# Kernel optimization log

Measured on AMD Instinct MI355X. Metric: run time of the kernel, lower is better.

## Reference

```python
import jax, jax.numpy as jnp
import numpy as np
from jax import lax

D_MODEL = 1024
N_HEADS = 16
D_HEAD = D_MODEL // N_HEADS  # 64
NB_FEAT = 266
CHUNK = 128
KERNEL_EPS = 1e-4
CAUSAL_EPS = 1e-6


def _gaussian_orthogonal_matrix(nb_rows, nb_cols, seed=0):
    # Performer gaussian_orthogonal_random_matrix, scaling=0:
    # stacked orthogonal blocks scaled by chi-distributed row norms.
    rng = np.random.default_rng(seed)
    blocks = []
    n_full = nb_rows // nb_cols + (1 if nb_rows % nb_cols else 0)
    for _ in range(n_full):
        g = rng.standard_normal((nb_cols, nb_cols))
        q_mat, _ = np.linalg.qr(g)
        blocks.append(q_mat.T)
    mat = np.concatenate(blocks, axis=0)[:nb_rows]
    multiplier = np.linalg.norm(rng.standard_normal((nb_rows, nb_cols)), axis=1)
    return jnp.asarray((multiplier[:, None] * mat).astype(np.float32))


def setup_inputs() -> dict:
    key = jax.random.key(0)
    ks = jax.random.split(key, 9)
    s = 1.0 / np.sqrt(D_MODEL)
    x = jax.random.normal(ks[0], (2, 4096, D_MODEL), dtype=jnp.float32)
    def lin(k):
        kw, kb = jax.random.split(k)
        W = jax.random.uniform(kw, (D_MODEL, D_MODEL), jnp.float32, -s, s)
        b = jax.random.uniform(kb, (D_MODEL,), jnp.float32, -s, s)
        return W, b
    Wq, bq = lin(ks[1]); Wk, bk = lin(ks[2]); Wv, bv = lin(ks[3]); Wo, bo = lin(ks[4])
    proj = _gaussian_orthogonal_matrix(NB_FEAT, D_HEAD)
    return {"x": x, "Wq": Wq, "bq": bq, "Wk": Wk, "bk": bk, "Wv": Wv, "bv": bv,
            "Wo": Wo, "bo": bo, "proj": proj}


def _softmax_kernel(data, proj, is_query):
    # Performer random-feature softmax kernel.
    data_normalizer = data.shape[-1] ** -0.25
    ratio = proj.shape[0] ** -0.5
    dn = data * data_normalizer  # [b,h,n,d]
    data_dash = jnp.einsum('bhnd,md->bhnm', dn, proj)
    diag = 0.5 * jnp.sum(dn * dn, axis=-1, keepdims=True)  # [b,h,n,1]
    if is_query:
        stab = jnp.max(data_dash, axis=-1, keepdims=True)
    else:
        stab = jnp.max(data_dash)
    return ratio * (jnp.exp(data_dash - diag - stab) + KERNEL_EPS)


def _causal_linear_attention(qp, kp, v, chunk_size):
    # Chunked O(n) causal linear attention (Performer noncuda variant).
    b, h, n, m = qp.shape
    d = v.shape[-1]
    nc = n // chunk_size
    qc = jnp.moveaxis(qp.reshape(b, h, nc, chunk_size, m), 2, 0)  # [nc,b,h,c,m]
    kc = jnp.moveaxis(kp.reshape(b, h, nc, chunk_size, m), 2, 0)
    vc = jnp.moveaxis(v.reshape(b, h, nc, chunk_size, d), 2, 0)   # [nc,b,h,c,d]

    def step(carry, inp):
        last_k, last_ctx = carry  # [b,h,m], [b,h,m,d]
        q, k, vv = inp
        k_cum = last_k[:, :, None, :] + jnp.cumsum(k, axis=-2)          # [b,h,c,m]
        D_inv = 1.0 / jnp.einsum('bhcm,bhcm->bhc', q, k_cum + CAUSAL_EPS)
        ctx = jnp.einsum('bhcm,bhcd->bhcmd', k, vv)                     # [b,h,c,m,d]
        ctx_cum = last_ctx[:, :, None, :, :] + jnp.cumsum(ctx, axis=2)
        out = jnp.einsum('bhcmd,bhcm,bhc->bhcd', ctx_cum, q, D_inv)
        return (k_cum[:, :, -1, :], ctx_cum[:, :, -1, :, :]), out

    carry0 = (jnp.zeros((b, h, m), qp.dtype), jnp.zeros((b, h, m, d), qp.dtype))
    _, outs = lax.scan(step, carry0, (qc, kc, vc))  # [nc,b,h,c,d]
    return jnp.moveaxis(outs, 0, 2).reshape(b, h, n, d)


def reference(x, Wq, bq, Wk, bk, Wv, bv, Wo, bo, proj):
    bsz, n, _ = x.shape
    def split_heads(t):
        return t.reshape(bsz, n, N_HEADS, D_HEAD).transpose(0, 2, 1, 3)  # [b,h,n,d]
    q = split_heads(x @ Wq.T + bq)
    k = split_heads(x @ Wk.T + bk)
    v = split_heads(x @ Wv.T + bv)
    q_prime = _softmax_kernel(q, proj, is_query=True)
    k_prime = _softmax_kernel(k, proj, is_query=False)
    attn = _causal_linear_attention(q_prime, k_prime, v, CHUNK)  # [b,h,n,d]
    attn = attn.transpose(0, 2, 1, 3).reshape(bsz, n, D_MODEL)
    return attn @ Wo.T + bo
```

## Files before the change

### kernel.cpp

```cpp
#include <hip/hip_runtime.h>

#define B_    2
#define NSEQ  4096
#define DM    1024
#define H_    16
#define DH    64
#define MF    266
#define MP    288
#define NROWS (B_*NSEQ)
#define NHROWS (B_*H_*NSEQ)
#define RATIO 0.06131393394849658f
#define DNORM 0.3535533905932738f
#define KEPS  1e-4f
#define CEPS  1e-6f

#define CH    128
#define NC    32
#define SROW  (65*MP)
#define SELEM (64*MP)

#define AS1 __attribute__((address_space(1)))
#define AS3 __attribute__((address_space(3)))

typedef unsigned short u16;
typedef unsigned int   u32;

typedef __bf16 bf16x8 __attribute__((ext_vector_type(8)));
typedef float  f32x4  __attribute__((ext_vector_type(4)));

__device__ __forceinline__ float b2f(u16 u){ u32 x = ((u32)u) << 16; return __builtin_bit_cast(float, x); }
__device__ __forceinline__ u16 f2b(float f){
    u32 x = __builtin_bit_cast(u32, f);
    u32 r = x + 0x7fffu + ((x >> 16) & 1u);
    return (u16)(r >> 16);
}
__device__ __forceinline__ u32 enc_max(float f){ u32 b = __builtin_bit_cast(u32, f); return (b & 0x80000000u) ? ~b : (b | 0x80000000u); }
__device__ __forceinline__ float dec_max(u32 u){ u32 b = (u & 0x80000000u) ? (u & 0x7fffffffu) : ~u; return __builtin_bit_cast(float, b); }

struct DetectArgs { const u32* p[10]; int nw[10]; };

__global__ void detect_all(DetectArgs a, u32* __restrict__ flags)
{
    __shared__ int cnt[256];
    int k = blockIdx.x;
    const u32* src = a.p[k];
    int nwords = a.nw[k];
    int t = threadIdx.x; int c = 0;
    for (int i = t; i < nwords; i += 256) {
        u32 w = src[i];
        int ea = (int)((w >> 7)  & 0xFF);
        int eb = (int)((w >> 23) & 0xFF);
        c += (ea >= 112 && ea <= 143) ? 1 : 0;
        c += (eb >= 112 && eb <= 143) ? 1 : 0;
    }
    cnt[t] = c; __syncthreads();
    for (int s = 128; s; s >>= 1) { if (t < s) cnt[t] += cnt[t + s]; __syncthreads(); }
    if (t == 0) flags[k] = (cnt[0] >= (nwords * 3) / 2) ? 1u : 0u;
}

__device__ __forceinline__ void conv8(const void* src, u16* dst, int i, u32 flag)
{
    if (flag) {
        *(uint4*)(dst + i) = *(const uint4*)((const u16*)src + i);
    } else {
        const float* s = (const float*)src + i;
        u16 tmp[8];
        #pragma unroll
        for (int j = 0; j < 8; ++j) tmp[j] = f2b(s[j]);
        *(uint4*)(dst + i) = *(uint4*)tmp;
    }
}

struct ConvAllArgs {
    const void* xs;    u16* xd;
    const void* wsrc[4]; u16* wdst[4];
    const void* bsrc[4]; u16* bdst[4];
    const void* pj;    u16* pjd;
    u32* gpart; u32* gmax;
    const u32* flags;
};

__global__ __launch_bounds__(256)
void conv_all(ConvAllArgs a)
{
    int blk = blockIdx.x, t = threadIdx.x;
    if (blk < 4096) {
        int i = blk * 2048 + t * 8;
        conv8(a.xs, a.xd, i, a.flags[0]);
    } else if (blk < 6144) {
        int r = blk - 4096; int w = r >> 9; int i = (r & 511) * 2048 + t * 8;
        conv8(a.wsrc[w], a.wdst[w], i, a.flags[1 + 2*w]);
    } else if (blk < 6148) {
        int w = blk - 6144; int i = t * 8;
        if (i < DM) conv8(a.bsrc[w], a.bdst[w], i, a.flags[2 + 2*w]);
    } else if (blk < 6157) {
        int i = (blk - 6148) * 2048 + t * 8;
        if (i < MF * DH) conv8(a.pj, a.pjd, i, a.flags[9]);
        else             *(uint4*)(a.pjd + i) = (uint4){0,0,0,0};
    } else {
        a.gpart[t] = 0u;
        if (t == 0) *a.gmax = 0u;
    }
}

#define GEMM_BODY(A_, Bm_, bm_, bn_, ACC_)                                    \
    const int K = DM;                                                          \
    __shared__ u16 As[128 * 64];                                               \
    __shared__ u16 Bs[128 * 64];                                               \
    int t = threadIdx.x;                                                       \
    int wave = t >> 6, lane = t & 63;                                          \
    int wm = wave >> 1, wn = wave & 1;                                         \
    int quad = lane >> 4, l16 = lane & 15;                                     \
    int rowc = lane >> 3;                                                      \
    int csrc = ((lane & 7) ^ rowc) * 8;                                        \
    int cA = wave * 4;                                                         \
    const u16* ap0 = A_  + (size_t)(bm_ + cA*8 + rowc) * K + csrc;             \
    const u16* bp0 = Bm_ + (size_t)(bn_ + cA*8 + rowc) * K + csrc;             \
    u16* lA = As + cA * 512;                                                   \
    u16* lB = Bs + cA * 512;                                                   \
    f32x4 ACC_[4][4];                                                          \
    _Pragma("unroll")                                                          \
    for (int i = 0; i < 4; ++i)                                                \
        _Pragma("unroll")                                                      \
        for (int j = 0; j < 4; ++j) ACC_[i][j] = (f32x4){0.f,0.f,0.f,0.f};     \
    for (int k0 = 0; k0 < K; k0 += 64) {                                       \
        _Pragma("unroll")                                                      \
        for (int j = 0; j < 4; ++j) {                                          \
            __builtin_amdgcn_global_load_lds((const AS1 void*)(ap0 + (size_t)j*8*K + k0), (AS3 void*)(lA + j*512), 16, 0, 0); \
            __builtin_amdgcn_global_load_lds((const AS1 void*)(bp0 + (size_t)j*8*K + k0), (AS3 void*)(lB + j*512), 16, 0, 0); \
        }                                                                      \
        __syncthreads();                                                       \
        _Pragma("unroll")                                                      \
        for (int ks = 0; ks < 2; ++ks) {                                       \
            bf16x8 af[4], bfr[4];                                              \
            int sw = ((((ks << 2) | quad) ^ (l16 & 7)) << 4);                  \
            _Pragma("unroll")                                                  \
            for (int i = 0; i < 4; ++i) {                                      \
                af[i]  = *(const bf16x8*)((const char*)As + (wm*64 + i*16 + l16)*128 + sw); \
                bfr[i] = *(const bf16x8*)((const char*)Bs + (wn*64 + i*16 + l16)*128 + sw); \
            }                                                                  \
            _Pragma("unroll")                                                  \
            for (int i = 0; i < 4; ++i)                                        \
                _Pragma("unroll")                                              \
                for (int j = 0; j < 4; ++j)                                    \
                    ACC_[i][j] = __builtin_amdgcn_mfma_f32_16x16x32_bf16(af[i], bfr[j], ACC_[i][j], 0, 0, 0); \
        }                                                                      \
        __syncthreads();                                                       \
    }

__global__ __launch_bounds__(256)
void gemm_qkv(const u16* __restrict__ A,
              const u16* __restrict__ Wqb, const u16* __restrict__ Wkb,
              const u16* __restrict__ Wvb,
              const u16* __restrict__ bqb, const u16* __restrict__ bkb,
              const u16* __restrict__ bvb,
              u16* __restrict__ Vb, float* __restrict__ Qf, float* __restrict__ Kf)
{
    int bid = blockIdx.x;
    int xcd = bid & 7, pos = bid >> 3;
    int lb  = xcd * 192 + pos;
    int z   = lb >> 9;
    int q   = lb & 511;
    int idx = q & 15, sg = q >> 4;
    int sgm = sg & 15, sgn = sg >> 4;
    int bm = (sgm*4 + (idx & 3)) * 128;
    int bn = (sgn*4 + (idx >> 2)) * 128;

    const u16* Bm   = (z == 0) ? Wvb : (z == 1) ? Wqb : Wkb;
    const u16* bias = (z == 0) ? bvb : (z == 1) ? bqb : bkb;
    GEMM_BODY(A, Bm, bm, bn, acc)
    float* Of = (z == 1) ? Qf : Kf;
    #pragma unroll
    for (int i = 0; i < 4; ++i) {
        #pragma unroll
        for (int j = 0; j < 4; ++j) {
            int col = bn + wn*64 + j*16 + l16;
            float bv = b2f(bias[col]);
            #pragma unroll
            for (int r = 0; r < 4; ++r) {
                int row = bm + wm*64 + i*16 + quad*4 + r;
                float v = acc[i][j][r] + bv;
                if (z == 0) Vb[(size_t)row * DM + col] = f2b(v);
                else        Of[(size_t)row * DM + col] = v;
            }
        }
    }
}

template<int OUT_BF16>
__global__ __launch_bounds__(256)
void gemm_nt(const u16* __restrict__ A, const u16* __restrict__ Bm,
             const u16* __restrict__ bias, void* __restrict__ C)
{
    int bm = blockIdx.x * 128, bn = blockIdx.y * 128;
    GEMM_BODY(A, Bm, bm, bn, acc)
    #pragma unroll
    for (int i = 0; i < 4; ++i) {
        #pragma unroll
        for (int j = 0; j < 4; ++j) {
            int col = bn + wn*64 + j*16 + l16;
            float bv = b2f(bias[col]);
            #pragma unroll
            for (int r = 0; r < 4; ++r) {
                int row = bm + wm*64 + i*16 + quad*4 + r;
                float v = acc[i][j][r] + bv;
                if (OUT_BF16) ((u16*)C)[(size_t)row * DM + col] = f2b(v);
                else          ((float*)C)[(size_t)row * DM + col] = v;
            }
        }
    }
}

__global__ __launch_bounds__(256)
void feat_qk(const float* __restrict__ Xq, const float* __restrict__ Xk,
             const u16* __restrict__ projP, u16* __restrict__ Qp,
             u16* __restrict__ Kp, u32* __restrict__ gpart,
             float* __restrict__ lstab)
{
    int blk = blockIdx.x;
    int isK = blk >> 11;
    int blk2 = blk & 2047;
    int bh = blk2 >> 6, nt = blk2 & 63;
    int b = bh >> 4, h = bh & 15;
    int n0 = nt * 64;
    int t = threadIdx.x;
    int lane = t & 63, w = t >> 6;
    int quad = lane >> 4, l16 = lane & 15;

    const float* X = isK ? Xk : Xq;
    u16* OutP = isK ? Kp : Qp;

    __shared__ uint4 smemU[2368];
    __shared__ float red4[4];
    u16* smem16 = (u16*)smemU;

    const float* xrow = X + ((size_t)(b * NSEQ + n0 + w*16 + l16)) * DM + h * DH;
    float va[2][8];
    #pragma unroll
    for (int ks = 0; ks < 2; ++ks) {
        float4 u0 = *(const float4*)(xrow + ks*32 + quad*8);
        float4 u1 = *(const float4*)(xrow + ks*32 + quad*8 + 4);
        va[ks][0]=u0.x; va[ks][1]=u0.y; va[ks][2]=u0.z; va[ks][3]=u0.w;
        va[ks][4]=u1.x; va[ks][5]=u1.y; va[ks][6]=u1.z; va[ks][7]=u1.w;
    }

    for (int i = t; i < 2304; i += 256) {
        int m = i >> 3, c = i & 7;
        uint4 v = *(const uint4*)(projP + m*64 + c*8);
        int dstb = m*128 + ((c*16) ^ ((m & 7) << 4));
        *(uint4*)((char*)smemU + dstb) = v;
    }

    bf16x8 ahi[2], alo[2];
    float sq = 0.f;
    #pragma unroll
    for (int ks = 0; ks < 2; ++ks) {
        #pragma unroll
        for (int i = 0; i < 8; ++i) {
            float v = va[ks][i] * DNORM;
            sq += v * v;
            u16 hb = f2b(v);
            float hv = b2f(hb);
            ahi[ks][i] = __builtin_bit_cast(__bf16, hb);
            alo[ks][i] = __builtin_bit_cast(__bf16, f2b(v - hv));
        }
    }
    sq += __shfl_xor(sq, 16, 64);
    sq += __shfl_xor(sq, 32, 64);
    float diag_my = 0.5f * sq;

    __syncthreads();

    f32x4 acc[18];
    #pragma unroll
    for (int j = 0; j < 18; ++j) acc[j] = (f32x4){0.f,0.f,0.f,0.f};
    #pragma unroll
    for (int j = 0; j < 18; ++j) {
        int m = j*16 + l16;
        #pragma unroll
        for (int ks = 0; ks < 2; ++ks) {
            int off = m*128 + (((quad*16) + ks*64) ^ ((m & 7) << 4));
            bf16x8 bf = *(const bf16x8*)((const char*)smemU + off);
            acc[j] = __builtin_amdgcn_mfma_f32_16x16x32_bf16(ahi[ks], bf, acc[j], 0, 0, 0);
            acc[j] = __builtin_amdgcn_mfma_f32_16x16x32_bf16(alo[ks], bf, acc[j], 0, 0, 0);
        }
    }

    float rmax[4];
    #pragma unroll
    for (int r = 0; r < 4; ++r) rmax[r] = -3.4e38f;
    #pragma unroll
    for (int j = 0; j < 16; ++j)
        #pragma unroll
        for (int r = 0; r < 4; ++r) rmax[r] = fmaxf(rmax[r], acc[j][r]);
    if (l16 < MF - 256) {
        #pragma unroll
        for (int r = 0; r < 4; ++r) rmax[r] = fmaxf(rmax[r], acc[16][r]);
    }
    #pragma unroll
    for (int s = 1; s < 16; s <<= 1)
        #pragma unroll
        for (int r = 0; r < 4; ++r)
            rmax[r] = fmaxf(rmax[r], __shfl_xor(rmax[r], s, 64));

    float stab_blk = 0.f;
    if (isK) {
        float wm2 = fmaxf(fmaxf(rmax[0], rmax[1]), fmaxf(rmax[2], rmax[3]));
        wm2 = fmaxf(wm2, __shfl_xor(wm2, 16, 64));
        wm2 = fmaxf(wm2, __shfl_xor(wm2, 32, 64));
        if (lane == 0) red4[w] = wm2;
        __syncthreads();
        stab_blk = fmaxf(fmaxf(red4[0], red4[1]), fmaxf(red4[2], red4[3]));
        if (t == 0) {
            atomicMax(&gpart[blk2 & 255], enc_max(stab_blk));
            lstab[blk2] = stab_blk;
        }
    }

    float dg[4];
    #pragma unroll
    for (int r = 0; r < 4; ++r) dg[r] = __shfl(diag_my, quad*4 + r, 64);

    __syncthreads();

    #pragma unroll
    for (int j = 0; j < 18; ++j) {
        int m = j*16 + l16;
        #pragma unroll
        for (int r = 0; r < 4; ++r) {
            float stab = isK ? stab_blk : rmax[r];
            float ex = __expf(acc[j][r] - dg[r] - stab);
            float val = isK ? (RATIO * ex) : (RATIO * (ex + KEPS));
            u16 ov = (m < MF) ? f2b(val) : (u16)0;
            smem16[(w*16 + quad*4 + r) * 296 + m] = ov;
        }
    }
    __syncthreads();

    u16* obase = OutP + ((size_t)bh * NSEQ + n0) * MP;
    for (int i = t; i < 2304; i += 256) {
        int row = i / 36, c = i - row * 36;
        *(uint4*)(obase + row*MP + c*8) = *(const uint4*)(smem16 + row*296 + c*8);
    }
}

__global__ void gmax_reduce(const u32* __restrict__ gpart, u32* __restrict__ gmax)
{
    __shared__ u32 r[256];
    int t = threadIdx.x;
    r[t] = gpart[t]; __syncthreads();
    for (int s = 128; s; s >>= 1) { if (t < s) r[t] = max(r[t], r[t + s]); __syncthreads(); }
    if (t == 0) *gmax = r[0];
}

__global__ __launch_bounds__(256)
void krescale(u16* __restrict__ Kp, const float* __restrict__ lstab,
              const u32* __restrict__ gmax)
{
    int gid = blockIdx.x * 256 + threadIdx.x;
    int row = gid / 36, cc = gid - row * 36;
    float g = dec_max(*gmax);
    float sc = __expf(lstab[row >> 6] - g);
    u16* p = Kp + (size_t)row * MP + cc*8;
    uint4 v = *(uint4*)p;
    u16* e = (u16*)&v;
    int m0 = cc * 8;
    #pragma unroll
    for (int j = 0; j < 8; ++j) {
        float kv = b2f(e[j]) * sc + RATIO * KEPS;
        e[j] = (m0 + j < MF) ? f2b(kv) : (u16)0;
    }
    *(uint4*)p = v;
}

__global__ __launch_bounds__(256)
void chunk_ST(const u16* __restrict__ Kp, const u16* __restrict__ Vb,
              u16* __restrict__ Sb, float* __restrict__ zf)
{
    int bhc = blockIdx.x;
    int bh = bhc >> 5, c = bhc & (NC - 1);
    int b = bh >> 4, h = bh & 15;
    int t = threadIdx.x, w = t >> 6, lane = t & 63;
    int quad = lane >> 4, l16 = lane & 15;
    int n0 = c * CH;

    __shared__ __align__(16) u16 KTs[288*40];
    __shared__ __align__(16) u16 VTs[80*136];

    {
        int d0 = (t >> 5) * 8, nb = (t & 31) * 4;
        const u16* vb2 = Vb + ((size_t)(b*NSEQ + n0 + nb)) * DM + h*DH + d0;
        uint4 r0 = *(const uint4*)(vb2);
        uint4 r1 = *(const uint4*)(vb2 + DM);
        uint4 r2 = *(const uint4*)(vb2 + 2*DM);
        uint4 r3 = *(const uint4*)(vb2 + 3*DM);
        const u32* a0 = (const u32*)&r0; const u32* a1 = (const u32*)&r1;
        const u32* a2 = (const u32*)&r2; const u32* a3 = (const u32*)&r3;
        #pragma unroll
        for (int e = 0; e < 8; ++e) {
            u32 w0 = a0[e>>1], w1 = a1[e>>1], w2 = a2[e>>1], w3 = a3[e>>1];
            u32 lo2, hi2;
            if (e & 1) { lo2 = (w0 >> 16) | (w1 & 0xFFFF0000u); hi2 = (w2 >> 16) | (w3 & 0xFFFF0000u); }
            else       { lo2 = (w0 & 0xFFFFu) | (w1 << 16);     hi2 = (w2 & 0xFFFFu) | (w3 << 16); }
            uint2 uu; uu.x = lo2; uu.y = hi2;
            *(uint2*)&VTs[(d0 + e)*136 + nb] = uu;
        }
        if (t < 128) VTs[64*136 + t] = 0x3F80u;
        if (t < 255) {
            int rr = 65 + t/17, cc2 = t - (t/17)*17;
            uint4 z4 = (uint4){0,0,0,0};
            *(uint4*)&VTs[rr*136 + cc2*8] = z4;
        }
    }

    f32x4 am[18], az[5];
    #pragma unroll
    for (int mt = 0; mt < 18; ++mt) am[mt] = (f32x4){0.f,0.f,0.f,0.f};
    #pragma unroll
    for (int j = 0; j < 5; ++j) az[j] = (f32x4){0.f,0.f,0.f,0.f};

    const u16* kbase = Kp + ((size_t)bh * NSEQ + n0) * MP;
    for (int qh = 0; qh < 4; ++qh) {
        __syncthreads();
        for (int i = t; i < 288; i += 256) {
            int nb4 = (i & 7) * 4, m0 = (i >> 3) * 8;
            const u16* kb = kbase + (size_t)(qh*32 + nb4) * MP + m0;
            uint4 r0 = *(const uint4*)(kb);
            uint4 r1 = *(const uint4*)(kb + MP);
            uint4 r2 = *(const uint4*)(kb + 2*MP);
            uint4 r3 = *(const uint4*)(kb + 3*MP);
            const u32* a0 = (const u32*)&r0; const u32* a1 = (const u32*)&r1;
            const u32* a2 = (const u32*)&r2; const u32* a3 = (const u32*)&r3;
            #pragma unroll
            for (int e = 0; e < 8; ++e) {
                u32 w0 = a0[e>>1], w1 = a1[e>>1], w2 = a2[e>>1], w3 = a3[e>>1];
                u32 lo2, hi2;
                if (e & 1) { lo2 = (w0 >> 16) | (w1 & 0xFFFF0000u); hi2 = (w2 >> 16) | (w3 & 0xFFFF0000u); }
                else       { lo2 = (w0 & 0xFFFFu) | (w1 << 16);     hi2 = (w2 & 0xFFFFu) | (w3 << 16); }
                uint2 uu; uu.x = lo2; uu.y = hi2;
                *(uint2*)&KTs[(m0 + e)*40 + nb4] = uu;
            }
        }
        __syncthreads();
        int nof = qh*32 + quad*8;
        bf16x8 aw = *(const bf16x8*)&VTs[(w*16 + l16)*136 + nof];
        bf16x8 a4 = *(const bf16x8*)&VTs[(64 + l16)*136 + nof];
        #pragma unroll
        for (int mt = 0; mt < 18; ++mt) {
            bf16x8 bk = *(const bf16x8*)&KTs[(mt*16 + l16)*40 + quad*8];
            am[mt] = __builtin_amdgcn_mfma_f32_16x16x32_bf16(aw, bk, am[mt], 0, 0, 0);
        }
        #pragma unroll
        for (int j = 0; j < 5; ++j) {
            int mtz = w + 4*j;
            if (mtz < 18) {
                bf16x8 bk = *(const bf16x8*)&KTs[(mtz*16 + l16)*40 + quad*8];
                az[j] = __builtin_amdgcn_mfma_f32_16x16x32_bf16(a4, bk, az[j], 0, 0, 0);
            }
        }
    }

    u16* sb = Sb + (size_t)bhc * SELEM;
    #pragma unroll
    for (int mt = 0; mt < 18; ++mt)
        #pragma unroll
        for (int r = 0; r < 4; ++r)
            sb[(size_t)(w*16 + quad*4 + r) * MP + mt*16 + l16] = f2b(am[mt][r]);
    if (quad == 0) {
        #pragma unroll
        for (int j = 0; j < 5; ++j) {
            int mtz = w + 4*j;
            if (mtz < 18) zf[(size_t)bhc * MP + mtz*16 + l16] = az[j][0];
        }
    }
}

__global__ __launch_bounds__(256)
void chunk_prefix(u16* __restrict__ Sb, float* __restrict__ zf)
{
    int gid = blockIdx.x * 256 + threadIdx.x;
    int bh = gid / SROW;
    int rem = gid - bh * SROW;
    float run = 0.f;
    if (rem < SELEM) {
        size_t base = (size_t)(bh * NC) * SELEM + rem;
        #pragma unroll 4
        for (int c2 = 0; c2 < NC; ++c2) {
            size_t o = base + (size_t)c2 * SELEM;
            float v = b2f(Sb[o]);
            Sb[o] = f2b(run);
            run += v;
        }
    } else {
        int m = rem - SELEM;
        size_t base = (size_t)(bh * NC) * MP + m;
        #pragma unroll 4
        for (int c2 = 0; c2 < NC; ++c2) {
            size_t o = base + (size_t)c2 * MP;
            float v = zf[o];
            zf[o] = run + CEPS;
            run += v;
        }
    }
}

__global__ __launch_bounds__(256)
void scan_mfma(const u16* __restrict__ Qp, const u16* __restrict__ Kp,
               const u16* __restrict__ Vb, const u16* __restrict__ Sb,
               const float* __restrict__ zf, u16* __restrict__ attn)
{
    int bhc = blockIdx.x;
    int bh = bhc >> 5, c = bhc & (NC - 1);
    int b = bh >> 4, h = bh & 15;
    int t = threadIdx.x, w = t >> 6, lane = t & 63;
    int quad = lane >> 4, l16 = lane & 15;
    int n0 = c * CH;
    int it0 = w, it1 = 7 - w;

    __shared__ __align__(16) u16 R1s[9472];
    __shared__ __align__(16) u16 R2s[17408];

    for (int i = t; i < 2176; i += 256) ((uint4*)R2s)[i] = (uint4){0,0,0,0};

    bf16x8 q0[9], q1[9];
    {
        const u16* qa = Qp + ((size_t)bh * NSEQ + n0 + it0*16 + l16) * MP + quad*8;
        const u16* qb = Qp + ((size_t)bh * NSEQ + n0 + it1*16 + l16) * MP + quad*8;
        #pragma unroll
        for (int s = 0; s < 9; ++s) {
            q0[s] = *(const bf16x8*)(qa + s*32);
            q1[s] = *(const bf16x8*)(qb + s*32);
        }
    }

    float denw0 = 0.f, denw1 = 0.f;
    const u16* kbase = Kp + ((size_t)bh * NSEQ + n0) * MP;

    for (int qt = 0; qt < 4; ++qt) {
        __syncthreads();
        for (int i = t; i < 1152; i += 256) {
            int rr = i / 36, cc = i - rr * 36;
            *(uint4*)&R1s[rr*296 + cc*8] =
                *(const uint4*)(kbase + (size_t)(qt*32 + rr) * MP + cc*8);
        }
        __syncthreads();
        #pragma unroll
        for (int jj = 0; jj < 2; ++jj) {
            int jt = qt*2 + jj;
            #pragma unroll
            for (int itx = 0; itx < 2; ++itx) {
                int it = itx ? it1 : it0;
                if (jt <= it) {
                    f32x4 acc = (f32x4){0.f,0.f,0.f,0.f};
                    #pragma unroll
                    for (int s = 0; s < 9; ++s) {
                        bf16x8 kf = *(const bf16x8*)&R1s[(jj*16 + l16)*296 + s*32 + quad*8];
                        acc = __builtin_amdgcn_mfma_f32_16x16x32_bf16(
                            kf, itx ? q1[s] : q0[s], acc, 0, 0, 0);
                    }
                    int ig = it*16 + l16;
                    float rs = 0.f;
                    #pragma unroll
                    for (int r = 0; r < 4; ++r) {
                        int jg = jt*16 + quad*4 + r;
                        float pv = (jg <= ig) ? acc[r] : 0.f;
                        rs += pv;
                        R2s[ig*136 + jg] = f2b(pv);
                    }
                    if (itx) denw1 += rs; else denw0 += rs;
                }
            }
        }
    }

    __syncthreads();
    {
        int d0 = (t >> 5) * 8, nb = (t & 31) * 4;
        const u16* vb2 = Vb + ((size_t)(b*NSEQ + n0 + nb)) * DM + h*DH + d0;
        uint4 r0 = *(const uint4*)(vb2);
        uint4 r1 = *(const uint4*)(vb2 + DM);
        uint4 r2 = *(const uint4*)(vb2 + 2*DM);
        uint4 r3 = *(const uint4*)(vb2 + 3*DM);
        const u32* a0 = (const u32*)&r0; const u32* a1 = (const u32*)&r1;
        const u32* a2 = (const u32*)&r2; const u32* a3 = (const u32*)&r3;
        #pragma unroll
        for (int e = 0; e < 8; ++e) {
            u32 w0 = a0[e>>1], w1 = a1[e>>1], w2 = a2[e>>1], w3 = a3[e>>1];
            u32 lo2, hi2;
            if (e & 1) { lo2 = (w0 >> 16) | (w1 & 0xFFFF0000u); hi2 = (w2 >> 16) | (w3 & 0xFFFF0000u); }
            else       { lo2 = (w0 & 0xFFFFu) | (w1 << 16);     hi2 = (w2 & 0xFFFFu) | (w3 << 16); }
            uint2 uu; uu.x = lo2; uu.y = hi2;
            *(uint2*)&R1s[(d0 + e)*136 + nb] = uu;
        }
    }
    __syncthreads();

    f32x4 pacc[2][4];
    #pragma unroll
    for (int i = 0; i < 2; ++i)
        #pragma unroll
        for (int j = 0; j < 4; ++j) pacc[i][j] = (f32x4){0.f,0.f,0.f,0.f};
    int ns0 = (it0 + 2) >> 1, ns1 = (it1 + 2) >> 1;
    #pragma unroll
    for (int ks = 0; ks < 4; ++ks) {
        bool u0 = ks < ns0, u1 = ks < ns1;
        bf16x8 p0 = {}, p1 = {};
        if (u0) p0 = *(const bf16x8*)&R2s[(it0*16 + l16)*136 + ks*32 + quad*8];
        if (u1) p1 = *(const bf16x8*)&R2s[(it1*16 + l16)*136 + ks*32 + quad*8];
        #pragma unroll
        for (int ct = 0; ct < 4; ++ct) {
            bf16x8 vf = *(const bf16x8*)&R1s[(ct*16 + l16)*136 + ks*32 + quad*8];
            if (u0) pacc[0][ct] = __builtin_amdgcn_mfma_f32_16x16x32_bf16(p0, vf, pacc[0][ct], 0, 0, 0);
            if (u1) pacc[1][ct] = __builtin_amdgcn_mfma_f32_16x16x32_bf16(p1, vf, pacc[1][ct], 0, 0, 0);
        }
    }

    f32x4 cacc[2][4];
    #pragma unroll
    for (int i = 0; i < 2; ++i)
        #pragma unroll
        for (int j = 0; j < 4; ++j) cacc[i][j] = (f32x4){0.f,0.f,0.f,0.f};
    const u16* sbw = Sb + (size_t)bhc * SELEM;
    #pragma unroll
    for (int p = 0; p < 2; ++p) {
        __syncthreads();
        for (int i = t; i < 1152; i += 256) {
            int rr = i / 36, cc = i - rr * 36;
            *(uint4*)&R1s[rr*296 + cc*8] =
                *(const uint4*)(sbw + (size_t)(p*32 + rr) * MP + cc*8);
        }
        __syncthreads();
        #pragma unroll
        for (int s = 0; s < 9; ++s)
            #pragma unroll
            for (int cl = 0; cl < 2; ++cl) {
                bf16x8 sf = *(const bf16x8*)&R1s[(cl*16 + l16)*296 + s*32 + quad*8];
                cacc[0][p*2 + cl] = __builtin_amdgcn_mfma_f32_16x16x32_bf16(q0[s], sf, cacc[0][p*2 + cl], 0, 0, 0);
                cacc[1][p*2 + cl] = __builtin_amdgcn_mfma_f32_16x16x32_bf16(q1[s], sf, cacc[1][p*2 + cl], 0, 0, 0);
            }
    }

    float dc0 = 0.f, dc1 = 0.f;
    {
        const float* zc = zf + (size_t)bhc * MP + quad*8;
        #pragma unroll
        for (int s = 0; s < 9; ++s) {
            f32x4 za = *(const f32x4*)(zc + s*32);
            f32x4 zb = *(const f32x4*)(zc + s*32 + 4);
            #pragma unroll
            for (int e = 0; e < 4; ++e) {
                dc0 += (float)q0[s][e] * za[e];
                dc0 += (float)q0[s][e+4] * zb[e];
                dc1 += (float)q1[s][e] * za[e];
                dc1 += (float)q1[s][e+4] * zb[e];
            }
        }
    }
    dc0 += __shfl_xor(dc0, 16, 64); dc0 += __shfl_xor(dc0, 32, 64);
    dc1 += __shfl_xor(dc1, 16, 64); dc1 += __shfl_xor(dc1, 32, 64);
    denw0 += __shfl_xor(denw0, 16, 64); denw0 += __shfl_xor(denw0, 32, 64);
    denw1 += __shfl_xor(denw1, 16, 64); denw1 += __shfl_xor(denw1, 32, 64);
    float den0 = denw0 + dc0, den1 = denw1 + dc1;

    u16* ab = attn + ((size_t)(b*NSEQ + n0)) * DM + h*DH;
    #pragma unroll
    for (int itx = 0; itx < 2; ++itx) {
        int it = itx ? it1 : it0;
        float dv = itx ? den1 : den0;
        #pragma unroll
        for (int r = 0; r < 4; ++r) {
            float deno = __shfl(dv, (lane & 48) + quad*4 + r, 64);
            int row = it*16 + quad*4 + r;
            #pragma unroll
            for (int ct = 0; ct < 4; ++ct) {
                float ov = (pacc[itx][ct][r] + cacc[itx][ct][r]) / deno;
                ab[(size_t)row * DM + ct*16 + l16] = f2b(ov);
            }
        }
    }
}

extern "C" void kernel_launch(void* const* d_in, const int* in_sizes, int n_in,
                              void* d_out, int out_size, void* d_ws, size_t ws_size,
                              hipStream_t stream)
{
    (void)n_in; (void)out_size; (void)ws_size;
    const void* x  = d_in[0];
    const void* Wq = d_in[1]; const void* bq = d_in[2];
    const void* Wk = d_in[3]; const void* bk = d_in[4];
    const void* Wv = d_in[5]; const void* bv = d_in[6];
    const void* Wo = d_in[7]; const void* bo = d_in[8];
    const void* proj = d_in[9];

    char* ws = (char*)d_ws;
    size_t off = 0;
    auto alloc = [&](size_t bytes) -> char* {
        char* p = ws + off; off += (bytes + 255) & ~(size_t)255; return p;
    };
    size_t qkfBytes = (size_t)NROWS * DM * 4;
    size_t sbBytes  = (size_t)(B_ * H_ * NC) * SELEM * 2;
    size_t zfBytes  = (size_t)(B_ * H_ * NC) * MP * 4;
    size_t ovBytes  = 2 * qkfBytes;
    if (sbBytes + zfBytes > ovBytes) ovBytes = sbBytes + zfBytes;
    char*  ov0  = alloc(ovBytes);
    float* QKf0 = (float*)ov0;
    float* QKf1 = (float*)(ov0 + qkfBytes);
    u16*   Sb   = (u16*)ov0;
    float* zfp  = (float*)(ov0 + sbBytes);
    u16*   Vb   = (u16*)alloc((size_t)NROWS * DM * 2);
    u16*   Qp   = (u16*)alloc((size_t)NHROWS * MP * 2);
    u16*   Kp   = (u16*)alloc((size_t)NHROWS * MP * 2);
    u16*   projC= (u16*)alloc((size_t)MP * DH * 2);
    u16*   Wqb  = (u16*)alloc((size_t)DM * DM * 2);
    u16*   Wkb  = (u16*)alloc((size_t)DM * DM * 2);
    u16*   Wvb  = (u16*)alloc((size_t)DM * DM * 2);
    u16*   Wob  = (u16*)alloc((size_t)DM * DM * 2);
    u16*   bqb  = (u16*)alloc(DM * 2);
    u16*   bkb  = (u16*)alloc(DM * 2);
    u16*   bvb  = (u16*)alloc(DM * 2);
    u16*   bob  = (u16*)alloc(DM * 2);
    u32*   flags= (u32*)alloc(16 * 4);
    u32*   gmax = (u32*)alloc(256);
    u32*   gpart= (u32*)alloc(256 * 4);
    float* lstab= (float*)alloc(2048 * 4);
    char*  xatt = alloc((size_t)NROWS * DM * 2);
    u16*   xb   = (u16*)xatt;
    u16*   attn = (u16*)xatt;

    DetectArgs da;
    for (int i = 0; i < 10; ++i) {
        int n = in_sizes[i];
        int nwords = n / 2; if (nwords > 4096) nwords = 4096;
        da.p[i] = (const u32*)d_in[i];
        da.nw[i] = nwords;
    }
    detect_all<<<10, 256, 0, stream>>>(da, flags);

    ConvAllArgs ca;
    ca.xs = x;  ca.xd = xb;
    ca.wsrc[0] = Wq; ca.wsrc[1] = Wk; ca.wsrc[2] = Wv; ca.wsrc[3] = Wo;
    ca.wdst[0] = Wqb; ca.wdst[1] = Wkb; ca.wdst[2] = Wvb; ca.wdst[3] = Wob;
    ca.bsrc[0] = bq; ca.bsrc[1] = bk; ca.bsrc[2] = bv; ca.bsrc[3] = bo;
    ca.bdst[0] = bqb; ca.bdst[1] = bkb; ca.bdst[2] = bvb; ca.bdst[3] = bob;
    ca.pj = proj; ca.pjd = projC;
    ca.gpart = gpart; ca.gmax = gmax; ca.flags = flags;
    conv_all<<<6158, 256, 0, stream>>>(ca);

    gemm_qkv<<<1536, 256, 0, stream>>>(xb, Wqb, Wkb, Wvb, bqb, bkb, bvb, Vb, QKf0, QKf1);

    feat_qk<<<4096, 256, 0, stream>>>(QKf0, QKf1, projC, Qp, Kp, gpart, lstab);
    gmax_reduce<<<1, 256, 0, stream>>>(gpart, gmax);
    krescale<<<18432, 256, 0, stream>>>(Kp, lstab, gmax);

    chunk_ST<<<B_ * H_ * NC, 256, 0, stream>>>(Kp, Vb, Sb, zfp);
    chunk_prefix<<<(B_ * H_ * SROW) / 256, 256, 0, stream>>>(Sb, zfp);
    scan_mfma<<<B_ * H_ * NC, 256, 0, stream>>>(Qp, Kp, Vb, Sb, zfp, attn);

    dim3 gg(NROWS / 128, DM / 128);
    gemm_nt<0><<<gg, 256, 0, stream>>>(attn, Wob, bob, d_out);
}
```

Baseline: 395.3 us.

## Fuse K rescale into chunk kernels and vectorize chunk prefix scan

Removes the standalone krescale pass over Kp. The global-max stabilizer scale and the eps offset are now applied on the fly inside chunk_ST during the transpose load, and inside scan_mfma algebraically as acc*scale + eps*sum(q). chunk_prefix is rewritten so each thread scans 8 bf16 or 4 float elements with vector loads, and f2b uses the native bf16 conversion. This saves a full read-modify-write of the K feature tensor. In exchange, scan_mfma now computes QK' from unrescaled bf16 values, which can shift rounding, and padded feature columns are no longer explicitly zeroed.

```diff
diff --git a/kernel.cpp b/kernel.cpp
--- a/kernel.cpp
+++ b/kernel.cpp
@@ -13,6 +13,7 @@
 #define DNORM 0.3535533905932738f
 #define KEPS  1e-4f
 #define CEPS  1e-6f
+#define RKC   (RATIO*KEPS)
 
 #define CH    128
 #define NC    32
@@ -30,9 +31,7 @@
 
 __device__ __forceinline__ float b2f(u16 u){ u32 x = ((u32)u) << 16; return __builtin_bit_cast(float, x); }
 __device__ __forceinline__ u16 f2b(float f){
-    u32 x = __builtin_bit_cast(u32, f);
-    u32 r = x + 0x7fffu + ((x >> 16) & 1u);
-    return (u16)(r >> 16);
+    return __builtin_bit_cast(u16, (__bf16)f);
 }
 __device__ __forceinline__ u32 enc_max(float f){ u32 b = __builtin_bit_cast(u32, f); return (b & 0x80000000u) ? ~b : (b | 0x80000000u); }
 __device__ __forceinline__ float dec_max(u32 u){ u32 b = (u & 0x80000000u) ? (u & 0x7fffffffu) : ~u; return __builtin_bit_cast(float, b); }
@@ -354,28 +353,9 @@
 }
 
 __global__ __launch_bounds__(256)
-void krescale(u16* __restrict__ Kp, const float* __restrict__ lstab,
-              const u32* __restrict__ gmax)
-{
-    int gid = blockIdx.x * 256 + threadIdx.x;
-    int row = gid / 36, cc = gid - row * 36;
-    float g = dec_max(*gmax);
-    float sc = __expf(lstab[row >> 6] - g);
-    u16* p = Kp + (size_t)row * MP + cc*8;
-    uint4 v = *(uint4*)p;
-    u16* e = (u16*)&v;
-    int m0 = cc * 8;
-    #pragma unroll
-    for (int j = 0; j < 8; ++j) {
-        float kv = b2f(e[j]) * sc + RATIO * KEPS;
-        e[j] = (m0 + j < MF) ? f2b(kv) : (u16)0;
-    }
-    *(uint4*)p = v;
-}
-
-__global__ __launch_bounds__(256)
 void chunk_ST(const u16* __restrict__ Kp, const u16* __restrict__ Vb,
-              u16* __restrict__ Sb, float* __restrict__ zf)
+              u16* __restrict__ Sb, float* __restrict__ zf,
+              const float* __restrict__ lstab, const u32* __restrict__ gmax)
 {
     int bhc = blockIdx.x;
     int bh = bhc >> 5, c = bhc & (NC - 1);
@@ -383,6 +363,10 @@
     int t = threadIdx.x, w = t >> 6, lane = t & 63;
     int quad = lane >> 4, l16 = lane & 15;
     int n0 = c * CH;
+
+    float gv = dec_max(*gmax);
+    float sA = __expf(lstab[bh*64 + c*2] - gv);
+    float sB = __expf(lstab[bh*64 + c*2 + 1] - gv);
 
     __shared__ __align__(16) u16 KTs[288*40];
     __shared__ __align__(16) u16 VTs[80*136];
@@ -421,6 +405,7 @@
 
     const u16* kbase = Kp + ((size_t)bh * NSEQ + n0) * MP;
     for (int qh = 0; qh < 4; ++qh) {
+        float sq4 = (qh < 2) ? sA : sB;
         __syncthreads();
         for (int i = t; i < 288; i += 256) {
             int nb4 = (i & 7) * 4, m0 = (i >> 3) * 8;
@@ -434,10 +419,14 @@
             #pragma unroll
             for (int e = 0; e < 8; ++e) {
                 u32 w0 = a0[e>>1], w1 = a1[e>>1], w2 = a2[e>>1], w3 = a3[e>>1];
-                u32 lo2, hi2;
-                if (e & 1) { lo2 = (w0 >> 16) | (w1 & 0xFFFF0000u); hi2 = (w2 >> 16) | (w3 & 0xFFFF0000u); }
-                else       { lo2 = (w0 & 0xFFFFu) | (w1 << 16);     hi2 = (w2 & 0xFFFFu) | (w3 << 16); }
-                uint2 uu; uu.x = lo2; uu.y = hi2;
+                u16 e0, e1, e2, e3;
+                if (e & 1) { e0 = (u16)(w0 >> 16); e1 = (u16)(w1 >> 16); e2 = (u16)(w2 >> 16); e3 = (u16)(w3 >> 16); }
+                else       { e0 = (u16)w0; e1 = (u16)w1; e2 = (u16)w2; e3 = (u16)w3; }
+                u16 f0 = f2b(b2f(e0)*sq4 + RKC);
+                u16 f1 = f2b(b2f(e1)*sq4 + RKC);
+                u16 f2 = f2b(b2f(e2)*sq4 + RKC);
+                u16 f3 = f2b(b2f(e3)*sq4 + RKC);
+                uint2 uu; uu.x = (u32)f0 | ((u32)f1 << 16); uu.y = (u32)f2 | ((u32)f3 << 16);
                 *(uint2*)&KTs[(m0 + e)*40 + nb4] = uu;
             }
         }
@@ -479,27 +468,38 @@
 void chunk_prefix(u16* __restrict__ Sb, float* __restrict__ zf)
 {
     int gid = blockIdx.x * 256 + threadIdx.x;
-    int bh = gid / SROW;
-    int rem = gid - bh * SROW;
-    float run = 0.f;
-    if (rem < SELEM) {
-        size_t base = (size_t)(bh * NC) * SELEM + rem;
-        #pragma unroll 4
+    if (gid < 32 * (SELEM/8)) {
+        int bh = gid / (SELEM/8);
+        int e8 = gid - bh * (SELEM/8);
+        size_t base = (size_t)(bh * NC) * SELEM + (size_t)e8 * 8;
+        float run[8];
+        #pragma unroll
+        for (int j = 0; j < 8; ++j) run[j] = 0.f;
         for (int c2 = 0; c2 < NC; ++c2) {
-            size_t o = base + (size_t)c2 * SELEM;
-            float v = b2f(Sb[o]);
-            Sb[o] = f2b(run);
-            run += v;
+            u16* p = Sb + base + (size_t)c2 * SELEM;
+            uint4 v = *(uint4*)p;
+            u16* e = (u16*)&v;
+            #pragma unroll
+            for (int j = 0; j < 8; ++j) {
+                float x = b2f(e[j]);
+                e[j] = f2b(run[j]);
+                run[j] += x;
+            }
+            *(uint4*)p = v;
         }
     } else {
-        int m = rem - SELEM;
-        size_t base = (size_t)(bh * NC) * MP + m;
-        #pragma unroll 4
+        int g2 = gid - 32 * (SELEM/8);
+        int bh = g2 / (MP/4);
+        int m4 = g2 - bh * (MP/4);
+        size_t base = (size_t)(bh * NC) * MP + (size_t)m4 * 4;
+        float run0 = 0.f, run1 = 0.f, run2 = 0.f, run3 = 0.f;
         for (int c2 = 0; c2 < NC; ++c2) {
-            size_t o = base + (size_t)c2 * MP;
-            float v = zf[o];
-            zf[o] = run + CEPS;
-            run += v;
+            float* p = zf + base + (size_t)c2 * MP;
+            float4 v = *(float4*)p;
+            float t0 = v.x, t1 = v.y, t2 = v.z, t3 = v.w;
+            v.x = run0 + CEPS; v.y = run1 + CEPS; v.z = run2 + CEPS; v.w = run3 + CEPS;
+            run0 += t0; run1 += t1; run2 += t2; run3 += t3;
+            *(float4*)p = v;
         }
     }
 }
@@ -507,7 +507,8 @@
 __global__ __launch_bounds__(256)
 void scan_mfma(const u16* __restrict__ Qp, const u16* __restrict__ Kp,
                const u16* __restrict__ Vb, const u16* __restrict__ Sb,
-               const float* __restrict__ zf, u16* __restrict__ attn)
+               const float* __restrict__ zf, const float* __restrict__ lstab,
+               const u32* __restrict__ gmax, u16* __restrict__ attn)
 {
     int bhc = blockIdx.x;
     int bh = bhc >> 5, c = bhc & (NC - 1);
@@ -520,6 +521,10 @@
     __shared__ __align__(16) u16 R1s[9472];
     __shared__ __align__(16) u16 R2s[17408];
 
+    float gv = dec_max(*gmax);
+    float sA = __expf(lstab[bh*64 + c*2] - gv);
+    float sB = __expf(lstab[bh*64 + c*2 + 1] - gv);
+
     for (int i = t; i < 2176; i += 256) ((uint4*)R2s)[i] = (uint4){0,0,0,0};
 
     bf16x8 q0[9], q1[9];
@@ -532,6 +537,15 @@
             q1[s] = *(const bf16x8*)(qb + s*32);
         }
     }
+
+    float qs0 = 0.f, qs1 = 0.f;
+    #pragma unroll
+    for (int s = 0; s < 9; ++s)
+        #pragma unroll
+        for (int e = 0; e < 8; ++e) { qs0 += (float)q0[s][e]; qs1 += (float)q1[s][e]; }
+    qs0 += __shfl_xor(qs0, 16, 64); qs0 += __shfl_xor(qs0, 32, 64);
+    qs1 += __shfl_xor(qs1, 16, 64); qs1 += __shfl_xor(qs1, 32, 64);
+    float rkq0 = RKC * qs0, rkq1 = RKC * qs1;
 
     float denw0 = 0.f, denw1 = 0.f;
     const u16* kbase = Kp + ((size_t)bh * NSEQ + n0) * MP;
@@ -547,6 +561,7 @@
         #pragma unroll
         for (int jj = 0; jj < 2; ++jj) {
             int jt = qt*2 + jj;
+            float sj = (jt < 4) ? sA : sB;
             #pragma unroll
             for (int itx = 0; itx < 2; ++itx) {
                 int it = itx ? it1 : it0;
@@ -559,11 +574,12 @@
                             kf, itx ? q1[s] : q0[s], acc, 0, 0, 0);
                     }
                     int ig = it*16 + l16;
+                    float rkq = itx ? rkq1 : rkq0;
                     float rs = 0.f;
                     #pragma unroll
                     for (int r = 0; r < 4; ++r) {
                         int jg = jt*16 + quad*4 + r;
-                        float pv = (jg <= ig) ? acc[r] : 0.f;
+                        float pv = (jg <= ig) ? (acc[r] * sj + rkq) : 0.f;
                         rs += pv;
                         R2s[ig*136 + jg] = f2b(pv);
                     }
@@ -750,11 +766,10 @@
 
     feat_qk<<<4096, 256, 0, stream>>>(QKf0, QKf1, projC, Qp, Kp, gpart, lstab);
     gmax_reduce<<<1, 256, 0, stream>>>(gpart, gmax);
-    krescale<<<18432, 256, 0, stream>>>(Kp, lstab, gmax);
-
-    chunk_ST<<<B_ * H_ * NC, 256, 0, stream>>>(Kp, Vb, Sb, zfp);
-    chunk_prefix<<<(B_ * H_ * SROW) / 256, 256, 0, stream>>>(Sb, zfp);
-    scan_mfma<<<B_ * H_ * NC, 256, 0, stream>>>(Qp, Kp, Vb, Sb, zfp, attn);
+
+    chunk_ST<<<B_ * H_ * NC, 256, 0, stream>>>(Kp, Vb, Sb, zfp, lstab, gmax);
+    chunk_prefix<<<297, 256, 0, stream>>>(Sb, zfp);
+    scan_mfma<<<B_ * H_ * NC, 256, 0, stream>>>(Qp, Kp, Vb, Sb, zfp, lstab, gmax, attn);
 
     dim3 gg(NROWS / 128, DM / 128);
     gemm_nt<0><<<gg, 256, 0, stream>>>(attn, Wob, bob, d_out);
```

Measured after the change: 397.4 us. No clear change (+0.5%).
